# Optimization experiments

Hardware: AMD Instinct MI355X
Metric: run time of the kernel (lower is better)

Reference implementation:

```python
import jax, jax.numpy as jnp
import numpy as np

H, DQS, DQP, DVS, DVP = 12, 16, 4, 16, 8
S_SCALAR = (3.0 * DQS) ** -0.5
S_POINT = (3.0 * DQP * (9.0 * 2.0 ** 0.5)) ** -0.5
S_PAIR = 3.0 ** -0.5
_OFF = np.cumsum([0, H * DQS, H * DQS, H * DVS, H * DQP * 3, H * DQP * 3, H * DVP * 3])


def _ln(x, g, b, eps=1e-5):
    mu = x.mean(-1, keepdims=True)
    var = x.var(-1, keepdims=True)
    return (x - mu) / jnp.sqrt(var + eps) * g + b


def setup_inputs() -> dict:
    B, N, D, PD = 2, 512, 384, 128
    key = jax.random.key(0)
    ks = jax.random.split(key, 12)
    node_feats = jax.random.normal(ks[0], (B, N, D), jnp.float32)
    pair_feats = jax.random.normal(ks[1], (B, N, N, PD), jnp.float32)
    mask = jnp.ones((B, N), dtype=bool)
    # random per-residue rigid frames (orthonormal rotations via QR)
    rot = jnp.linalg.qr(jax.random.normal(ks[2], (B, N, 3, 3), jnp.float32))[0]
    trans = jax.random.normal(ks[3], (B, N, 3), jnp.float32)
    dim_qkv = int(_OFF[-1])             # 1152
    dim_out = H * (PD + DVS + 4 * DVP)  # 2112
    s = 0.02
    p = dict(
        ln_s_g=jnp.ones((D,)), ln_s_b=jnp.zeros((D,)),
        ln_p_g=jnp.ones((PD,)), ln_p_b=jnp.zeros((PD,)),
        w_pair_bias=s * jax.random.normal(ks[4], (PD, H), jnp.float32),
        w_qkv=s * jax.random.normal(ks[5], (D, dim_qkv), jnp.float32),
        point_weights=jnp.full((1, H, 1, 1), float(np.log(np.e - 1.0)), jnp.float32),
        w_out=s * jax.random.normal(ks[6], (dim_out, D), jnp.float32),
        b_out=jnp.zeros((D,)),
        ln_t_g=jnp.ones((D,)), ln_t_b=jnp.zeros((D,)),
        w_ff1=s * jax.random.normal(ks[7], (D, 4 * D), jnp.float32),
        b_ff1=jnp.zeros((4 * D,)),
        w_ff2=s * jax.random.normal(ks[8], (4 * D, D), jnp.float32),
        b_ff2=jnp.zeros((D,)),
    )
    return dict(node_feats=node_feats, pair_feats=pair_feats, mask=mask,
                rot=rot, trans=trans, **p)


def reference(node_feats, pair_feats, mask, rot, trans,
              ln_s_g, ln_s_b, ln_p_g, ln_p_b, w_pair_bias, w_qkv,
              point_weights, w_out, b_out,
              ln_t_g, ln_t_b, w_ff1, b_ff1, w_ff2, b_ff2):
    b, n, d = node_feats.shape
    x = _ln(node_feats, ln_s_g, ln_s_b)
    p = _ln(pair_feats, ln_p_g, ln_p_b)
    pair_bias = jnp.einsum('bijd,dh->bhij', p, w_pair_bias)
    qkv = x @ w_qkv  # (b,n,1152)

    def heads(t, dh):
        return t.reshape(b, n, H, dh).transpose(0, 2, 1, 3)  # b h n d

    q_s = heads(qkv[..., _OFF[0]:_OFF[1]], DQS)
    k_s = heads(qkv[..., _OFF[1]:_OFF[2]], DQS)
    v_s = heads(qkv[..., _OFF[2]:_OFF[3]], DVS)

    def to_pts(t, dp):
        pts = t.reshape(b, n, H * dp, 3)
        # rigid apply: R_i @ x + t_i (global frame)
        pts = jnp.einsum('bnxy,bnpy->bnpx', rot, pts) + trans[:, :, None, :]
        return pts.reshape(b, n, H, dp, 3).transpose(0, 2, 1, 3, 4)  # b h n d 3

    q_p = to_pts(qkv[..., _OFF[3]:_OFF[4]], DQP)
    k_p = to_pts(qkv[..., _OFF[4]:_OFF[5]], DQP)
    v_p = to_pts(qkv[..., _OFF[5]:_OFF[6]], DVP)

    scalar_logits = jnp.einsum('bhid,bhjd->bhij', q_s, k_s)
    # dist attn: -sum_{d,c} (q-k)^2, expanded to avoid (b,h,n,n,d,3) intermediate
    qq = jnp.sum(q_p * q_p, axis=(-1, -2))
    kk = jnp.sum(k_p * k_p, axis=(-1, -2))
    qk = jnp.einsum('bhidc,bhjdc->bhij', q_p, k_p)
    point_logits = -(qq[..., :, None] + kk[..., None, :] - 2.0 * qk)
    point_logits = point_logits * jax.nn.softplus(point_weights)

    neg = jnp.finfo(node_feats.dtype).min
    pm = mask[:, None, :, None] & mask[:, None, None, :]  # b 1 i j
    scalar_logits = jnp.where(pm, scalar_logits, neg)
    point_logits = jnp.where(pm, point_logits, neg)
    pair_bias = jnp.where(pm, pair_bias, neg)

    logits = S_SCALAR * scalar_logits + S_POINT * point_logits + S_PAIR * pair_bias
    attn = jax.nn.softmax(logits, axis=-1)

    out_s = jnp.einsum('bhij,bhjd->bhid', attn, v_s)
    out_pair = jnp.einsum('bhij,bijd->bhid', attn, p)
    out_p = jnp.einsum('bhij,bhjdc->bhidc', attn, v_p)
    # rigid inverse: R_i^T (x - t_i) back to local frame
    pts = out_p.transpose(0, 2, 1, 3, 4).reshape(b, n, H * DVP, 3)
    pts = jnp.einsum('bnyx,bnpy->bnpx', rot, pts - trans[:, :, None, :])
    out_p = pts.reshape(b, n, H, DVP, 3)
    pnorm = jnp.sqrt(jnp.sum(out_p * out_p, axis=-1) + 1e-8)  # safe_norm

    cat = jnp.concatenate([
        out_s.transpose(0, 2, 1, 3).reshape(b, n, H * DVS),
        out_p.reshape(b, n, H * DVP * 3),
        pnorm.reshape(b, n, H * DVP),
        out_pair.transpose(0, 2, 1, 3).reshape(b, n, -1),
    ], axis=-1)
    attn_out = cat @ w_out + b_out

    # residuals + transition (dropout=0 -> identity). Note: transition is
    # applied to attn_out (pre-residual), exactly as in the torch forward.
    node1 = attn_out + node_feats
    t = _ln(attn_out, ln_t_g, ln_t_b)
    t = jax.nn.gelu(t @ w_ff1 + b_ff1) @ w_ff2 + b_ff2
    return t + node1
```

## Files before the change

### kernel.cpp

```cpp
#include <hip/hip_runtime.h>
#include <hip/hip_bf16.h>
#include <math.h>

typedef __hip_bfloat16 bf16;
typedef _Float16 f16;
typedef unsigned short ushort_t;
typedef ushort_t ushort8 __attribute__((ext_vector_type(8)));
typedef ushort_t us4 __attribute__((ext_vector_type(4)));
typedef short bf16x8 __attribute__((ext_vector_type(8)));
typedef f16 f16x8 __attribute__((ext_vector_type(8)));
typedef float f32x4 __attribute__((ext_vector_type(4)));

constexpr float S_SCALAR = 0.14433756729740643f;
constexpr float S_POINT  = 0.08091531528f;
constexpr float S_PAIR   = 0.5773502691896258f;

__device__ inline short f2bfs(float x) {
  return (short)__builtin_bit_cast(unsigned short, __float2bfloat16(x));
}
__device__ inline ushort_t f2bfu(float x) {
  return (ushort_t)__builtin_bit_cast(unsigned short, __float2bfloat16(x));
}
__device__ inline ushort_t f2hu(float x) {
  return __builtin_bit_cast(ushort_t, (f16)x);
}
__device__ inline float h2f(ushort_t u) {
  return (float)__builtin_bit_cast(f16, u);
}

__device__ inline float gelu_tanh(float x) {
  float c = 0.7978845608028654f * (x + 0.044715f * x * x * x);
  return 0.5f * x * (1.f + tanhf(c));
}

__global__ __launch_bounds__(128) void ln384_kernel(
    const float* __restrict__ in, const float* __restrict__ g,
    const float* __restrict__ b, float* __restrict__ out)
{
  int row = blockIdx.x;
  const float* x = in + (size_t)row * 384;
  int t = threadIdx.x;
  float v[3]; float s = 0.f, s2 = 0.f;
#pragma unroll
  for (int i = 0; i < 3; i++) { v[i] = x[t + 128 * i]; s += v[i]; s2 += v[i] * v[i]; }
  for (int o = 32; o; o >>= 1) { s += __shfl_down(s, o); s2 += __shfl_down(s2, o); }
  __shared__ float sh[4];
  int wid = t >> 6, lane = t & 63;
  if (lane == 0) { sh[wid] = s; sh[2 + wid] = s2; }
  __syncthreads();
  s = sh[0] + sh[1]; s2 = sh[2] + sh[3];
  float mean = s * (1.f / 384.f);
  float var = s2 * (1.f / 384.f) - mean * mean;
  float rstd = rsqrtf(fmaxf(var, 0.f) + 1e-5f);
  float* orow = out + (size_t)row * 384;
#pragma unroll
  for (int i = 0; i < 3; i++) {
    int c = t + 128 * i;
    orow[c] = (v[i] - mean) * rstd * g[c] + b[c];
  }
}

__global__ __launch_bounds__(256) void prep_all_kernel(
    const float* __restrict__ w_qkv, const float* __restrict__ w_out,
    const float* __restrict__ w_ff1, const float* __restrict__ w_ff2,
    ushort_t* __restrict__ wqkvT, ushort_t* __restrict__ woutT,
    ushort_t* __restrict__ wff1T, ushort_t* __restrict__ wff2T,
    const float* __restrict__ g, const float* __restrict__ bb,
    const float* __restrict__ wpb, ushort_t* __restrict__ gwbT,
    float* __restrict__ gsbs,
    const float* __restrict__ node, const float* __restrict__ ln_s_g,
    const float* __restrict__ ln_s_b, float* __restrict__ xout)
{
  __shared__ float shmem[2048];
  int bid = blockIdx.x;
  int t = threadIdx.x;
  if (bid < 2376) {
    const float* src; ushort_t* dst; int K, N, bx, by;
    if (bid < 432)       { src = w_qkv; dst = wqkvT; K = 384;  N = 1152; bx = bid % 36;          by = bid / 36; }
    else if (bid < 1224) { src = w_out; dst = woutT; K = 2112; N = 384;  bx = (bid - 432) % 12;  by = (bid - 432) / 12; }
    else if (bid < 1800) { src = w_ff1; dst = wff1T; K = 384;  N = 1536; bx = (bid - 1224) % 48; by = (bid - 1224) / 48; }
    else                 { src = w_ff2; dst = wff2T; K = 1536; N = 384;  bx = (bid - 1800) % 12; by = (bid - 1800) / 12; }
    float (&tile)[32][33] = *reinterpret_cast<float (*)[32][33]>(shmem);
    int n0 = bx * 32, k0 = by * 32;
    int c = t & 31, r4 = (t >> 5) * 4;
#pragma unroll
    for (int i = 0; i < 4; i++)
      tile[r4 + i][c] = src[(size_t)(k0 + r4 + i) * N + n0 + c];
    __syncthreads();
#pragma unroll
    for (int i = 0; i < 4; i++)
      dst[(size_t)(n0 + r4 + i) * K + k0 + c] = f2bfu(tile[c][r4 + i]);
    return;
  }
  if (bid == 2376) {
    for (int idx = t; idx < 2048; idx += 256) {
      int h = idx >> 7, c = idx & 127;
      float v = (h < 12) ? g[c] * wpb[c * 12 + h] : 0.f;
      bf16 r = __float2bfloat16(v);
      gwbT[idx] = __builtin_bit_cast(unsigned short, r);
      shmem[idx] = __bfloat162float(r);
    }
    __syncthreads();
    if (t < 16) {
      float s = 0.f;
      for (int c = 0; c < 128; c++) s += shmem[t * 128 + c];
      gsbs[t] = s;
    } else if (t < 32) {
      int h = t - 16;
      float s = 0.f;
      if (h < 12) for (int c = 0; c < 128; c++) s = fmaf(bb[c], wpb[c * 12 + h], s);
// ... 76 lines not shown
      acc[1][1] = __builtin_amdgcn_mfma_f32_16x16x32_bf16(af1, bf1, acc[1][1], 0, 0, 0);
    }
    __syncthreads();
  }
#pragma unroll
  for (int mf = 0; mf < 2; mf++) {
#pragma unroll
    for (int nf = 0; nf < 2; nf++) {
      int nn = n0 + wn + nf * 16 + lr;
      float bv = bias ? bias[nn] : 0.f;
#pragma unroll
      for (int e = 0; e < 4; e++) {
        int m = m0 + wm + mf * 16 + lk * 4 + e;
        float v = acc[mf][nf][e] + bv;
        if (EPI == 1) v = gelu_tanh(v);
        if (EPI == 2) v += r1[(size_t)m * Nn + nn] + r2[(size_t)m * Nn + nn];
        C[(size_t)m * Nn + nn] = v;
      }
    }
  }
}

template <int EPI>
__global__ __launch_bounds__(256) void gemm_mfma_m32_kernel(
    const float* __restrict__ A, const ushort_t* __restrict__ BT,
    const float* __restrict__ bias, const float* __restrict__ r1,
    const float* __restrict__ r2, float* __restrict__ C,
    int M, int Nn, int K)
{
  __shared__ ushort_t As[32][72];
  __shared__ ushort_t Bs[64][72];
  int t = threadIdx.x;
  int w = t >> 6, l = t & 63;
  int m0 = blockIdx.y * 32, n0 = blockIdx.x * 64;
  int wm = (w & 1) * 16, wn = (w >> 1) * 32;
  int lr = l & 15, lk = l >> 4;
  int ar = t >> 3, ac = (t & 7) * 8;
  int br = t >> 2, bc = (t & 3) * 16;
  f32x4 acc[2];
  acc[0] = (f32x4){0.f, 0.f, 0.f, 0.f};
  acc[1] = (f32x4){0.f, 0.f, 0.f, 0.f};

  for (int k0 = 0; k0 < K; k0 += 64) {
    const float* Ar = A + (size_t)(m0 + ar) * K + k0 + ac;
    float4 a0 = *(const float4*)(Ar + 0);
    float4 a1 = *(const float4*)(Ar + 4);
    ushort8 u;
    u[0] = f2bfu(a0.x); u[1] = f2bfu(a0.y); u[2] = f2bfu(a0.z); u[3] = f2bfu(a0.w);
    u[4] = f2bfu(a1.x); u[5] = f2bfu(a1.y); u[6] = f2bfu(a1.z); u[7] = f2bfu(a1.w);
    *(ushort8*)&As[ar][ac] = u;
    const ushort_t* Br = BT + (size_t)(n0 + br) * K + k0 + bc;
    *(ushort8*)&Bs[br][bc] = *(const ushort8*)(Br + 0);
    *(ushort8*)&Bs[br][bc + 8] = *(const ushort8*)(Br + 8);
    __syncthreads();
#pragma unroll
    for (int kk = 0; kk < 2; kk++) {
      bf16x8 af = *(const bf16x8*)&As[wm + lr][kk * 32 + lk * 8];
      bf16x8 bf0 = *(const bf16x8*)&Bs[wn + lr][kk * 32 + lk * 8];
      bf16x8 bf1 = *(const bf16x8*)&Bs[wn + 16 + lr][kk * 32 + lk * 8];
      acc[0] = __builtin_amdgcn_mfma_f32_16x16x32_bf16(af, bf0, acc[0], 0, 0, 0);
      acc[1] = __builtin_amdgcn_mfma_f32_16x16x32_bf16(af, bf1, acc[1], 0, 0, 0);
    }
    __syncthreads();
  }
#pragma unroll
  for (int nf = 0; nf < 2; nf++) {
    int nn = n0 + wn + nf * 16 + lr;
    float bv = bias ? bias[nn] : 0.f;
#pragma unroll
    for (int e = 0; e < 4; e++) {
      int m = m0 + wm + lk * 4 + e;
      float v = acc[nf][e] + bv;
      if (EPI == 1) v = gelu_tanh(v);
      if (EPI == 2) v += r1[(size_t)m * Nn + nn] + r2[(size_t)m * Nn + nn];
      C[(size_t)m * Nn + nn] = v;
    }
  }
}

__global__ __launch_bounds__(256) void qkv_post_kernel(
    const float* __restrict__ qkv, const float* __restrict__ rot,
    const float* __restrict__ trans, const float* __restrict__ pw,
    f16* __restrict__ qhat, f16* __restrict__ khat,
    float* __restrict__ kkb, ushort_t* __restrict__ vT)
{
  int bh = blockIdx.x;
  int b = bh / 12, h = bh - b * 12;
  int role = blockIdx.y >> 1;
  int j = (blockIdx.y & 1) * 256 + threadIdx.x;
  int bn = b * 512 + j;
  const float* row = qkv + (size_t)bn * 1152;
  float R[9];
#pragma unroll
  for (int k = 0; k < 9; k++) R[k] = rot[bn * 9 + k];
  float T0 = trans[bn * 3], T1 = trans[bn * 3 + 1], T2 = trans[bn * 3 + 2];
  if (role == 0) {
    float sp = log1pf(__expf(pw[h]));
    float c1 = 2.f * S_POINT * sp;
    f16* qh = qhat + ((size_t)bh * 512 + j) * 32;
#pragma unroll
    for (int d = 0; d < 16; d++) qh[d] = (f16)(S_SCALAR * row[h * 16 + d]);
#pragma unroll
    for (int p = 0; p < 4; p++) {
      int base = 576 + (h * 4 + p) * 3;
      float x = row[base], y = row[base + 1], z = row[base + 2];
      qh[16 + p * 3 + 0] = (f16)(c1 * (R[0] * x + R[1] * y + R[2] * z + T0));
      qh[16 + p * 3 + 1] = (f16)(c1 * (R[3] * x + R[4] * y + R[5] * z + T1));
      qh[16 + p * 3 + 2] = (f16)(c1 * (R[6] * x + R[7] * y + R[8] * z + T2));
    }
#pragma unroll
    for (int d = 28; d < 32; d++) qh[d] = (f16)0.f;
  } else if (role == 1) {
    f16* kh = khat + ((size_t)bh * 512 + j) * 32;
#pragma unroll
    for (int d = 0; d < 16; d++) kh[d] = (f16)(row[192 + h * 16 + d]);
    float kksum = 0.f;
#pragma unroll
    for (int p = 0; p < 4; p++) {
      int base = 720 + (h * 4 + p) * 3;
      float x = row[base], y = row[base + 1], z = row[base + 2];
      float gx = R[0] * x + R[1] * y + R[2] * z + T0;
      float gy = R[3] * x + R[4] * y + R[5] * z + T1;
      float gz = R[6] * x + R[7] * y + R[8] * z + T2;
      kh[16 + p * 3 + 0] = (f16)gx; kh[16 + p * 3 + 1] = (f16)gy; kh[16 + p * 3 + 2] = (f16)gz;
      kksum = fmaf(gx, gx, kksum); kksum = fmaf(gy, gy, kksum); kksum = fmaf(gz, gz, kksum);
    }
#pragma unroll
    for (int d = 28; d < 32; d++) kh[d] = (f16)0.f;
    kkb[(size_t)bh * 512 + j] = kksum;
  } else {
    ushort_t* vt = vT + (size_t)bh * 40 * 512;
#pragma unroll
    for (int c = 0; c < 16; c++) vt[c * 512 + j] = f2hu(row[384 + h * 16 + c]);
#pragma unroll
    for (int p = 0; p < 8; p++) {
      int base = 864 + (h * 8 + p) * 3;
      float x = row[base], y = row[base + 1], z = row[base + 2];
      vt[(16 + p * 3 + 0) * 512 + j] = f2hu(R[0] * x + R[1] * y + R[2] * z + T0);
      vt[(16 + p * 3 + 1) * 512 + j] = f2hu(R[3] * x + R[4] * y + R[5] * z + T1);
      vt[(16 + p * 3 + 2) * 512 + j] = f2hu(R[6] * x + R[7] * y + R[8] * z + T2);
    }
  }
}

__global__ __launch_bounds__(256) void pair_bias_kernel(
    const float* __restrict__ pair, const ushort_t* __restrict__ gwbT,
    const float* __restrict__ gsbs, const float* __restrict__ g,
    const float* __restrict__ bb, ushort_t* __restrict__ bias,
    f16* __restrict__ pnT)
{
  __shared__ ushort_t tile[128][136];
  int t = threadIdx.x;
  int wv = t >> 6, l = t & 63;
  int lr = l & 15, lk = l >> 4;
  size_t rid0 = (size_t)blockIdx.x * 128 + (size_t)wv * 32;

  bf16x8 bfrag[4];
#pragma unroll
  for (int kc = 0; kc < 4; kc++) {
    const ushort_t* gp = gwbT + lr * 128 + kc * 32 + lk * 8;
    us4 q0 = *(const us4*)gp;
    us4 q1 = *(const us4*)(gp + 4);
    bfrag[kc][0] = (short)q0[0]; bfrag[kc][1] = (short)q0[1];
    bfrag[kc][2] = (short)q0[2]; bfrag[kc][3] = (short)q0[3];
    bfrag[kc][4] = (short)q1[0]; bfrag[kc][5] = (short)q1[1];
    bfrag[kc][6] = (short)q1[2]; bfrag[kc][7] = (short)q1[3];
  }

  const float* p0 = pair + (rid0 + lr) * 128 + lk * 8;
  f32x4 acc0 = {0.f, 0.f, 0.f, 0.f}, acc1 = {0.f, 0.f, 0.f, 0.f};
  float s0 = 0.f, s20 = 0.f, s1 = 0.f, s21 = 0.f;
#pragma unroll
  for (int kc = 0; kc < 4; kc++) {
    float4 u0 = *(const float4*)(p0 + kc * 32);
    float4 u1 = *(const float4*)(p0 + kc * 32 + 4);
    float4 w0 = *(const float4*)(p0 + 2048 + kc * 32);
    float4 w1 = *(const float4*)(p0 + 2048 + kc * 32 + 4);
    s0 += u0.x + u0.y + u0.z + u0.w + u1.x + u1.y + u1.z + u1.w;
    s20 = fmaf(u0.x, u0.x, s20); s20 = fmaf(u0.y, u0.y, s20);
    s20 = fmaf(u0.z, u0.z, s20); s20 = fmaf(u0.w, u0.w, s20);
    s20 = fmaf(u1.x, u1.x, s20); s20 = fmaf(u1.y, u1.y, s20);
    s20 = fmaf(u1.z, u1.z, s20); s20 = fmaf(u1.w, u1.w, s20);
    s1 += w0.x + w0.y + w0.z + w0.w + w1.x + w1.y + w1.z + w1.w;
    s21 = fmaf(w0.x, w0.x, s21); s21 = fmaf(w0.y, w0.y, s21);
    s21 = fmaf(w0.z, w0.z, s21); s21 = fmaf(w0.w, w0.w, s21);
    s21 = fmaf(w1.x, w1.x, s21); s21 = fmaf(w1.y, w1.y, s21);
    s21 = fmaf(w1.z, w1.z, s21); s21 = fmaf(w1.w, w1.w, s21);
    bf16x8 a0, a1;
    a0[0] = f2bfs(u0.x); a0[1] = f2bfs(u0.y); a0[2] = f2bfs(u0.z); a0[3] = f2bfs(u0.w);
    a0[4] = f2bfs(u1.x); a0[5] = f2bfs(u1.y); a0[6] = f2bfs(u1.z); a0[7] = f2bfs(u1.w);
    a1[0] = f2bfs(w0.x); a1[1] = f2bfs(w0.y); a1[2] = f2bfs(w0.z); a1[3] = f2bfs(w0.w);
    a1[4] = f2bfs(w1.x); a1[5] = f2bfs(w1.y); a1[6] = f2bfs(w1.z); a1[7] = f2bfs(w1.w);
    acc0 = __builtin_amdgcn_mfma_f32_16x16x32_bf16(a0, bfrag[kc], acc0, 0, 0, 0);
    acc1 = __builtin_amdgcn_mfma_f32_16x16x32_bf16(a1, bfrag[kc], acc1, 0, 0, 0);
  }
  s0 += __shfl_xor(s0, 16);  s0 += __shfl_xor(s0, 32);
  s20 += __shfl_xor(s20, 16); s20 += __shfl_xor(s20, 32);
  s1 += __shfl_xor(s1, 16);  s1 += __shfl_xor(s1, 32);
  s21 += __shfl_xor(s21, 16); s21 += __shfl_xor(s21, 32);
  float mean0 = s0 * (1.f / 128.f);
  float rstd0 = rsqrtf(fmaxf(s20 * (1.f / 128.f) - mean0 * mean0, 0.f) + 1e-5f);
  float mean1 = s1 * (1.f / 128.f);
  float rstd1 = rsqrtf(fmaxf(s21 * (1.f / 128.f) - mean1 * mean1, 0.f) + 1e-5f);

  int jl_u = wv * 32 + lr, jl_w = wv * 32 + 16 + lr;
#pragma unroll
  for (int kc = 0; kc < 4; kc++) {
    int c0 = kc * 32 + lk * 8;
    float4 u0 = *(const float4*)(p0 + kc * 32);
    float4 u1 = *(const float4*)(p0 + kc * 32 + 4);
    float4 w0 = *(const float4*)(p0 + 2048 + kc * 32);
    float4 w1 = *(const float4*)(p0 + 2048 + kc * 32 + 4);
    float4 g0 = *(const float4*)(g + c0);
    float4 g1 = *(const float4*)(g + c0 + 4);
    float4 b0 = *(const float4*)(bb + c0);
    float4 b1 = *(const float4*)(bb + c0 + 4);
    float uu[8] = {u0.x, u0.y, u0.z, u0.w, u1.x, u1.y, u1.z, u1.w};
    float ww[8] = {w0.x, w0.y, w0.z, w0.w, w1.x, w1.y, w1.z, w1.w};
    float gg[8] = {g0.x, g0.y, g0.z, g0.w, g1.x, g1.y, g1.z, g1.w};
    float bv[8] = {b0.x, b0.y, b0.z, b0.w, b1.x, b1.y, b1.z, b1.w};
#pragma unroll
    for (int e = 0; e < 8; e++) {
      int c = c0 + e;
      int sw = ((c >> 3) & 7) << 4;
      tile[c][jl_u ^ sw] = f2hu(fmaf((uu[e] - mean0) * rstd0, gg[e], bv[e]));
      tile[c][jl_w ^ sw] = f2hu(fmaf((ww[e] - mean1) * rstd1, gg[e], bv[e]));
    }
  }
  __syncthreads();
  {
    int slab = blockIdx.x >> 2;
    int j0blk = (blockIdx.x & 3) * 128;
    ushort_t* dstb = (ushort_t*)pnT + (size_t)slab * 65536 + j0blk;
#pragma unroll
    for (int it = 0; it < 8; it++) {
      int idx = t + 256 * it;
      int c = idx >> 4, o = idx & 15;
      int sw = ((c >> 3) & 7) << 4;
      ushort8 v = *(const ushort8*)&tile[c][(o * 8) ^ sw];
      *(ushort8*)(dstb + (size_t)c * 512 + o * 8) = v;
    }
  }

  float gsum = gsbs[lr], bsum = gsbs[16 + lr];
  int b = (int)(rid0 >> 18);
  int i = (int)((rid0 >> 9) & 511);
  int j0 = (int)(rid0 & 511);
  us4 pk0, pk1;
#pragma unroll
  for (int e = 0; e < 4; e++) {
    int r = lk * 4 + e;
    float m0 = __shfl(mean0, r), rs0 = __shfl(rstd0, r);
    float m1 = __shfl(mean1, r), rs1 = __shfl(rstd1, r);
    pk0[e] = f2hu(rs0 * (acc0[e] - m0 * gsum) + bsum);
    pk1[e] = f2hu(rs1 * (acc1[e] - m1 * gsum) + bsum);
  }
  if (lr < 12) {
    ushort_t* dst = bias + ((size_t)(b * 12 + lr) * 512 + i) * 512 + j0 + lk * 4;
    *(us4*)dst = pk0;
    *(us4*)(dst + 16) = pk1;
  }
}

__global__ __launch_bounds__(256, 1) void attn_kernel(
    const f16* __restrict__ qhat, const f16* __restrict__ khat,
    const float* __restrict__ kkb, const ushort_t* __restrict__ bias,
    const float* __restrict__ pw, ushort_t* __restrict__ attn)
{
  int i0 = blockIdx.x * 64;
  int bh = blockIdx.y;
  int b = bh / 12, h = bh - b * 12;
  int t = threadIdx.x;
  int w = t >> 6, l = t & 63, lr = l & 15, lk = l >> 4;
  float spp = S_POINT * log1pf(__expf(pw[h]));
  int i = i0 + w * 16 + lr;
  f16x8 bfrag = *(const f16x8*)(qhat + ((size_t)bh * 512 + i) * 32 + lk * 8);
  const f16* kbase = khat + (size_t)bh * 512 * 32;
  const float* kkrow = kkb + (size_t)bh * 512;
  const ushort_t* brow = bias + ((size_t)bh * 512 + i) * 512;
  float lg[32][4];
  float pmax = -3.0e38f;
#pragma unroll
  for (int jt = 0; jt < 32; jt++) {
    f16x8 afrag = *(const f16x8*)(kbase + (size_t)(jt * 16 + lr) * 32 + lk * 8);
    f32x4 c = {0.f, 0.f, 0.f, 0.f};
    c = __builtin_amdgcn_mfma_f32_16x16x32_f16(afrag, bfrag, c, 0, 0, 0);
    us4 bq = *(const us4*)(brow + jt * 16 + lk * 4);
    float4 kq = *(const float4*)(kkrow + jt * 16 + lk * 4);
    float kk4[4] = {kq.x, kq.y, kq.z, kq.w};
#pragma unroll
    for (int e = 0; e < 4; e++) {
      float lv = c[e] + S_PAIR * h2f(bq[e]) - spp * kk4[e];
      lg[jt][e] = lv;
      pmax = fmaxf(pmax, lv);
    }
  }
  pmax = fmaxf(pmax, __shfl_xor(pmax, 16));
  pmax = fmaxf(pmax, __shfl_xor(pmax, 32));
  float ssum = 0.f;
#pragma unroll
  for (int jt = 0; jt < 32; jt++)
#pragma unroll
    for (int e = 0; e < 4; e++) {
      float p = __expf(lg[jt][e] - pmax);
      lg[jt][e] = p;
      ssum += p;
    }
  ssum += __shfl_xor(ssum, 16);
  ssum += __shfl_xor(ssum, 32);
  float inv = 1.f / ssum;
  ushort_t* arow = attn + ((size_t)(b * 512 + i) * 12 + h) * 512;
#pragma unroll
  for (int jt = 0; jt < 32; jt++) {
    us4 o;
#pragma unroll
    for (int e = 0; e < 4; e++) o[e] = f2hu(lg[jt][e] * inv);
    *(us4*)(arow + jt * 16 + lk * 4) = o;
  }
}

__global__ __launch_bounds__(256) void sv_gemm_kernel(
    const ushort_t* __restrict__ attn, const ushort_t* __restrict__ vT,
    float* __restrict__ svraw)
{
  int i0 = blockIdx.x * 64;
  int bh = blockIdx.y;
  int b = bh / 12, h = bh - b * 12;
  __shared__ ushort_t As_[64][72];
  __shared__ ushort_t Bs_[48][72];
  int t = threadIdx.x;
  int w = t >> 6, l = t & 63, lr = l & 15, lk = l >> 4;
  int ai = t >> 2, as = (t & 3) * 16;
  const ushort_t* vbase = vT + (size_t)bh * 40 * 512;
  f32x4 acc[3];
#pragma unroll
  for (int n = 0; n < 3; n++) acc[n] = (f32x4){0.f, 0.f, 0.f, 0.f};

  for (int jt = 0; jt < 8; jt++) {
    int jb = jt * 64;
    size_t aoff = ((size_t)(b * 512 + i0 + ai) * 12 + h) * 512 + jb + as;
    ushort8 a0 = *(const ushort8*)(attn + aoff);
    ushort8 a1 = *(const ushort8*)(attn + aoff + 8);
    *(ushort8*)&As_[ai][as] = a0;
    *(ushort8*)&As_[ai][as + 8] = a1;
    for (int idx = t; idx < 384; idx += 256) {
      int c = idx >> 3, j8 = (idx & 7) * 8;
      ushort8 v = {0, 0, 0, 0, 0, 0, 0, 0};
      if (c < 40) v = *(const ushort8*)(vbase + (size_t)c * 512 + jb + j8);
      *(ushort8*)&Bs_[c][j8] = v;
    }
    __syncthreads();
#pragma unroll
    for (int kk = 0; kk < 2; kk++) {
      f16x8 af = *(const f16x8*)&As_[w * 16 + lr][kk * 32 + lk * 8];
#pragma unroll
      for (int n = 0; n < 3; n++) {
        f16x8 bf_ = *(const f16x8*)&Bs_[n * 16 + lr][kk * 32 + lk * 8];
        acc[n] = __builtin_amdgcn_mfma_f32_16x16x32_f16(af, bf_, acc[n], 0, 0, 0);
      }
    }
    __syncthreads();
  }
#pragma unroll
  for (int n = 0; n < 3; n++) {
    int c = n * 16 + lr;
    if (c < 40) {
#pragma unroll
      for (int e = 0; e < 4; e++) {
        int i = i0 + w * 16 + lk * 4 + e;
        svraw[(size_t)(b * 512 + i) * 480 + h * 40 + c] = acc[n][e];
      }
    }
  }
}

__global__ __launch_bounds__(256) void pair_out_kernel(
    const ushort_t* __restrict__ attn, const f16* __restrict__ pnT,
    const float* __restrict__ svraw, const float* __restrict__ rot,
    const float* __restrict__ trans, float* __restrict__ cat)
{
  int bn = blockIdx.x;
  int t = threadIdx.x;
  const float* sv = svraw + (size_t)bn * 480;
  float* crow = cat + (size_t)bn * 2112;
  if (t < 192) {
    int h2 = t >> 4, d = t & 15;
    crow[t] = sv[h2 * 40 + d];
    if (t < 96) {
      int h3 = t >> 3, dp = t & 7;
      float T0 = trans[bn * 3], T1 = trans[bn * 3 + 1], T2 = trans[bn * 3 + 2];
      const float* R = rot + bn * 9;
      float px = sv[h3 * 40 + 16 + dp * 3 + 0] - T0;
      float py = sv[h3 * 40 + 16 + dp * 3 + 1] - T1;
      float pz = sv[h3 * 40 + 16 + dp * 3 + 2] - T2;
      float lx = R[0] * px + R[3] * py + R[6] * pz;
      float ly = R[1] * px + R[4] * py + R[7] * pz;
      float lz = R[2] * px + R[5] * py + R[8] * pz;
      crow[192 + h3 * 24 + dp * 3 + 0] = lx;
      crow[192 + h3 * 24 + dp * 3 + 1] = ly;
      crow[192 + h3 * 24 + dp * 3 + 2] = lz;
      crow[480 + h3 * 8 + dp] = sqrtf(lx * lx + ly * ly + lz * lz + 1e-8f);
    }
  }
  int w = t >> 6, l = t & 63, lr = l & 15, lk = l >> 4;
  const ushort_t* arow = attn + (size_t)bn * 12 * 512;
  int ar = (lr < 12) ? lr : 11;
  const f16* slab = pnT + (size_t)bn * 65536;
  int n0 = w * 32;
  f32x4 acc0 = {0.f, 0.f, 0.f, 0.f}, acc1 = {0.f, 0.f, 0.f, 0.f};
#pragma unroll
  for (int ks = 0; ks < 16; ks++) {
    int kb = ks * 32 + lk * 8;
    f16x8 af = *(const f16x8*)((const f16*)arow + (size_t)ar * 512 + kb);
    f16x8 b0 = *(const f16x8*)(slab + (size_t)(n0 + lr) * 512 + kb);
    f16x8 b1 = *(const f16x8*)(slab + (size_t)(n0 + 16 + lr) * 512 + kb);
    acc0 = __builtin_amdgcn_mfma_f32_16x16x32_f16(af, b0, acc0, 0, 0, 0);
    acc1 = __builtin_amdgcn_mfma_f32_16x16x32_f16(af, b1, acc1, 0, 0, 0);
  }
#pragma unroll
  for (int e = 0; e < 4; e++) {
    int hh = lk * 4 + e;
    if (hh < 12) {
      crow[576 + hh * 128 + n0 + lr] = acc0[e];
      crow[576 + hh * 128 + n0 + 16 + lr] = acc1[e];
    }
  }
}

extern "C" void kernel_launch(void* const* d_in, const int* in_sizes, int n_in,
                              void* d_out, int out_size, void* d_ws, size_t ws_size,
                              hipStream_t stream)
{
  const float* node   = (const float*)d_in[0];
  const float* pair   = (const float*)d_in[1];
  const float* rot    = (const float*)d_in[3];
  const float* trans  = (const float*)d_in[4];
  const float* ln_s_g = (const float*)d_in[5];
  const float* ln_s_b = (const float*)d_in[6];
  const float* ln_p_g = (const float*)d_in[7];
  const float* ln_p_b = (const float*)d_in[8];
  const float* wpb    = (const float*)d_in[9];
  const float* w_qkv  = (const float*)d_in[10];
  const float* pw     = (const float*)d_in[11];
  const float* w_out  = (const float*)d_in[12];
  const float* b_out  = (const float*)d_in[13];
  const float* ln_t_g = (const float*)d_in[14];
  const float* ln_t_b = (const float*)d_in[15];
  const float* w_ff1  = (const float*)d_in[16];
  const float* b_ff1  = (const float*)d_in[17];
  const float* w_ff2  = (const float*)d_in[18];
  const float* b_ff2  = (const float*)d_in[19];
  float* out = (float*)d_out;
  float* ws = (float*)d_ws;

  float* qkv    = ws;
  float* x      = ws + 1179648;
  float* tn     = x;
  float* ao     = ws + 1572864;
  float* svraw  = ws + 1966080;
  ushort_t* biasb = (ushort_t*)(ws + 2457600);
  float* cat    = ws + 2457600;
  ushort_t* attnb = (ushort_t*)(ws + 5603328);
  float* gb     = ws + 5603328;
  ushort_t* gwbT = (ushort_t*)(ws + 8749056);
  float* gsbs   = ws + 8750080;
  ushort_t* wqkvT = (ushort_t*)(ws + 8750112);
  ushort_t* woutT = (ushort_t*)(ws + 8971296);
  ushort_t* wff1T = (ushort_t*)(ws + 9376800);
  ushort_t* wff2T = (ushort_t*)(ws + 9671712);
  f16* qhat     = (f16*)(ws + 9966624);
  f16* khat     = (f16*)(ws + 10163232);
  float* kkb    = ws + 10359840;
  ushort_t* vT  = (ushort_t*)(ws + 10372128);
  f16* pnT      = (f16*)(ws + 10617888);

  prep_all_kernel<<<2889, 256, 0, stream>>>(w_qkv, w_out, w_ff1, w_ff2,
      wqkvT, woutT, wff1T, wff2T, ln_p_g, ln_p_b, wpb, gwbT, gsbs,
      node, ln_s_g, ln_s_b, x);
  gemm_mfma_kernel<0><<<dim3(18, 16), 256, 0, stream>>>(x, wqkvT, nullptr, nullptr, nullptr, qkv, 1024, 1152, 384);
  qkv_post_kernel<<<dim3(24, 6), 256, 0, stream>>>(qkv, rot, trans, pw, qhat, khat, kkb, vT);
  pair_bias_kernel<<<4096, 256, 0, stream>>>(pair, gwbT, gsbs, ln_p_g, ln_p_b, biasb, pnT);
  attn_kernel<<<dim3(8, 24), 256, 0, stream>>>(qhat, khat, kkb, biasb, pw, attnb);
  sv_gemm_kernel<<<dim3(8, 24), 256, 0, stream>>>(attnb, vT, svraw);
  pair_out_kernel<<<1024, 256, 0, stream>>>(attnb, pnT, svraw, rot, trans, cat);
  gemm_mfma_m32_kernel<0><<<dim3(6, 32), 256, 0, stream>>>(cat, woutT, b_out, nullptr, nullptr, ao, 1024, 384, 2112);
  ln384_kernel<<<1024, 128, 0, stream>>>(ao, ln_t_g, ln_t_b, tn);
  gemm_mfma_kernel<1><<<dim3(24, 16), 256, 0, stream>>>(tn, wff1T, b_ff1, nullptr, nullptr, gb, 1024, 1536, 384);
  gemm_mfma_m32_kernel<2><<<dim3(6, 32), 256, 0, stream>>>(gb, wff2T, b_ff2, ao, node, out, 1024, 384, 1536);
}
```

Measured before the change: 587.6 us.

## Fuse pair LayerNorm, pair bias, softmax and pair-output into one per-row kernel

Replaces the pair_bias, attention and pair_out kernels with a single kernel per (b,i) row. It layer-normalises the pair slab, computes the bias with MFMA, does the q·k logits with fdot2 and an online softmax over four 128-column chunks, then accumulates attn·pair from shared memory. The -spp·|k|² term is folded into qhat/khat as an extra dot-product element, so the kkb buffer goes away. This avoids writing and re-reading the bias and the transposed normalized pair tensor (pnT) in global memory. In exchange it adds many block-wide syncs per chunk and stores |k|² in fp16, which risks precision loss.

```diff
diff --git a/kernel.cpp b/kernel.cpp
--- a/kernel.cpp
+++ b/kernel.cpp
@@ -9,7 +9,9 @@
 typedef ushort_t us4 __attribute__((ext_vector_type(4)));
 typedef short bf16x8 __attribute__((ext_vector_type(8)));
 typedef f16 f16x8 __attribute__((ext_vector_type(8)));
+typedef f16 f16x2 __attribute__((ext_vector_type(2)));
 typedef float f32x4 __attribute__((ext_vector_type(4)));
+typedef unsigned int u32x4 __attribute__((ext_vector_type(4)));
 
 constexpr float S_SCALAR = 0.14433756729740643f;
 constexpr float S_POINT  = 0.08091531528f;
@@ -26,6 +28,15 @@
 }
 __device__ inline float h2f(ushort_t u) {
   return (float)__builtin_bit_cast(f16, u);
+}
+__device__ inline float fdot2f(unsigned a, unsigned b, float c) {
+#if __has_builtin(__builtin_amdgcn_fdot2)
+  return __builtin_amdgcn_fdot2(__builtin_bit_cast(f16x2, a),
+                                __builtin_bit_cast(f16x2, b), c, false);
+#else
+  f16x2 av = __builtin_bit_cast(f16x2, a), bv = __builtin_bit_cast(f16x2, b);
+  return c + (float)av[0] * (float)bv[0] + (float)av[1] * (float)bv[1];
+#endif
 }
 
 __device__ inline float gelu_tanh(float x) {
@@ -268,7 +279,7 @@
     const float* __restrict__ qkv, const float* __restrict__ rot,
     const float* __restrict__ trans, const float* __restrict__ pw,
     f16* __restrict__ qhat, f16* __restrict__ khat,
-    float* __restrict__ kkb, ushort_t* __restrict__ vT)
+    ushort_t* __restrict__ vT)
 {
   int bh = blockIdx.x;
   int b = bh / 12, h = bh - b * 12;
@@ -283,6 +294,7 @@
   if (role == 0) {
     float sp = log1pf(__expf(pw[h]));
     float c1 = 2.f * S_POINT * sp;
+    float spp = S_POINT * sp;
     f16* qh = qhat + ((size_t)bh * 512 + j) * 32;
 #pragma unroll
     for (int d = 0; d < 16; d++) qh[d] = (f16)(S_SCALAR * row[h * 16 + d]);
@@ -294,8 +306,8 @@
       qh[16 + p * 3 + 1] = (f16)(c1 * (R[3] * x + R[4] * y + R[5] * z + T1));
       qh[16 + p * 3 + 2] = (f16)(c1 * (R[6] * x + R[7] * y + R[8] * z + T2));
     }
-#pragma unroll
-    for (int d = 28; d < 32; d++) qh[d] = (f16)0.f;
+    qh[28] = (f16)(-spp);
+    qh[29] = (f16)0.f; qh[30] = (f16)0.f; qh[31] = (f16)0.f;
   } else if (role == 1) {
     f16* kh = khat + ((size_t)bh * 512 + j) * 32;
 #pragma unroll
@@ -311,9 +323,8 @@
       kh[16 + p * 3 + 0] = (f16)gx; kh[16 + p * 3 + 1] = (f16)gy; kh[16 + p * 3 + 2] = (f16)gz;
       kksum = fmaf(gx, gx, kksum); kksum = fmaf(gy, gy, kksum); kksum = fmaf(gz, gz, kksum);
     }
-#pragma unroll
-    for (int d = 28; d < 32; d++) kh[d] = (f16)0.f;
-    kkb[(size_t)bh * 512 + j] = kksum;
+    kh[28] = (f16)kksum;
+    kh[29] = (f16)0.f; kh[30] = (f16)0.f; kh[31] = (f16)0.f;
   } else {
     ushort_t* vt = vT + (size_t)bh * 40 * 512;
 #pragma unroll
@@ -329,18 +340,32 @@
   }
 }
 
-__global__ __launch_bounds__(256) void pair_bias_kernel(
+__global__ __launch_bounds__(256) void mega_kernel(
     const float* __restrict__ pair, const ushort_t* __restrict__ gwbT,
     const float* __restrict__ gsbs, const float* __restrict__ g,
-    const float* __restrict__ bb, ushort_t* __restrict__ bias,
-    f16* __restrict__ pnT)
+    const float* __restrict__ bb, const f16* __restrict__ qhat,
+    const f16* __restrict__ khat, ushort_t* __restrict__ attnb,
+    float* __restrict__ cat)
 {
   __shared__ ushort_t tile[128][136];
+  __shared__ ushort_t Ps[16][520];
+  __shared__ ushort_t bias_s[16][136];
+  __shared__ unsigned qhat_u[12][16];
+  __shared__ float red_s[2][6][4];
+  __shared__ float m_s[16], l_s[16], r_s[16], invl_s[16];
+  __shared__ float mhist_s[4][16], cf_s[4][16];
+
+  int bn = blockIdx.x;
+  int b = bn >> 9, i = bn & 511;
   int t = threadIdx.x;
-  int wv = t >> 6, l = t & 63;
-  int lr = l & 15, lk = l >> 4;
-  size_t rid0 = (size_t)blockIdx.x * 128 + (size_t)wv * 32;
-
+  int wv = t >> 6, ln = t & 63, lr = ln & 15, lk = ln >> 4;
+
+  if (t < 16) { m_s[t] = -3.0e38f; l_s[t] = 0.f; r_s[t] = 1.f; }
+  for (int idx = t; idx < 4 * 520; idx += 256) Ps[12 + idx / 520][idx % 520] = 0;
+  if (t < 192) {
+    int h = t >> 4, d4 = t & 15;
+    qhat_u[h][d4] = ((const unsigned*)qhat)[((size_t)(b * 12 + h) * 512 + i) * 16 + d4];
+  }
   bf16x8 bfrag[4];
 #pragma unroll
   for (int kc = 0; kc < 4; kc++) {
@@ -352,156 +377,180 @@
     bfrag[kc][4] = (short)q1[0]; bfrag[kc][5] = (short)q1[1];
     bfrag[kc][6] = (short)q1[2]; bfrag[kc][7] = (short)q1[3];
   }
-
-  const float* p0 = pair + (rid0 + lr) * 128 + lk * 8;
-  f32x4 acc0 = {0.f, 0.f, 0.f, 0.f}, acc1 = {0.f, 0.f, 0.f, 0.f};
-  float s0 = 0.f, s20 = 0.f, s1 = 0.f, s21 = 0.f;
-#pragma unroll
-  for (int kc = 0; kc < 4; kc++) {
-    float4 u0 = *(const float4*)(p0 + kc * 32);
-    float4 u1 = *(const float4*)(p0 + kc * 32 + 4);
-    float4 w0 = *(const float4*)(p0 + 2048 + kc * 32);
-    float4 w1 = *(const float4*)(p0 + 2048 + kc * 32 + 4);
-    s0 += u0.x + u0.y + u0.z + u0.w + u1.x + u1.y + u1.z + u1.w;
-    s20 = fmaf(u0.x, u0.x, s20); s20 = fmaf(u0.y, u0.y, s20);
-    s20 = fmaf(u0.z, u0.z, s20); s20 = fmaf(u0.w, u0.w, s20);
-    s20 = fmaf(u1.x, u1.x, s20); s20 = fmaf(u1.y, u1.y, s20);
-    s20 = fmaf(u1.z, u1.z, s20); s20 = fmaf(u1.w, u1.w, s20);
-    s1 += w0.x + w0.y + w0.z + w0.w + w1.x + w1.y + w1.z + w1.w;
-    s21 = fmaf(w0.x, w0.x, s21); s21 = fmaf(w0.y, w0.y, s21);
-    s21 = fmaf(w0.z, w0.z, s21); s21 = fmaf(w0.w, w0.w, s21);
-    s21 = fmaf(w1.x, w1.x, s21); s21 = fmaf(w1.y, w1.y, s21);
-    s21 = fmaf(w1.z, w1.z, s21); s21 = fmaf(w1.w, w1.w, s21);
-    bf16x8 a0, a1;
-    a0[0] = f2bfs(u0.x); a0[1] = f2bfs(u0.y); a0[2] = f2bfs(u0.z); a0[3] = f2bfs(u0.w);
-    a0[4] = f2bfs(u1.x); a0[5] = f2bfs(u1.y); a0[6] = f2bfs(u1.z); a0[7] = f2bfs(u1.w);
-    a1[0] = f2bfs(w0.x); a1[1] = f2bfs(w0.y); a1[2] = f2bfs(w0.z); a1[3] = f2bfs(w0.w);
-    a1[4] = f2bfs(w1.x); a1[5] = f2bfs(w1.y); a1[6] = f2bfs(w1.z); a1[7] = f2bfs(w1.w);
-    acc0 = __builtin_amdgcn_mfma_f32_16x16x32_bf16(a0, bfrag[kc], acc0, 0, 0, 0);
-    acc1 = __builtin_amdgcn_mfma_f32_16x16x32_bf16(a1, bfrag[kc], acc1, 0, 0, 0);
-  }
-  s0 += __shfl_xor(s0, 16);  s0 += __shfl_xor(s0, 32);
-  s20 += __shfl_xor(s20, 16); s20 += __shfl_xor(s20, 32);
-  s1 += __shfl_xor(s1, 16);  s1 += __shfl_xor(s1, 32);
-  s21 += __shfl_xor(s21, 16); s21 += __shfl_xor(s21, 32);
-  float mean0 = s0 * (1.f / 128.f);
-  float rstd0 = rsqrtf(fmaxf(s20 * (1.f / 128.f) - mean0 * mean0, 0.f) + 1e-5f);
-  float mean1 = s1 * (1.f / 128.f);
-  float rstd1 = rsqrtf(fmaxf(s21 * (1.f / 128.f) - mean1 * mean1, 0.f) + 1e-5f);
-
-  int jl_u = wv * 32 + lr, jl_w = wv * 32 + 16 + lr;
-#pragma unroll
-  for (int kc = 0; kc < 4; kc++) {
-    int c0 = kc * 32 + lk * 8;
-    float4 u0 = *(const float4*)(p0 + kc * 32);
-    float4 u1 = *(const float4*)(p0 + kc * 32 + 4);
-    float4 w0 = *(const float4*)(p0 + 2048 + kc * 32);
-    float4 w1 = *(const float4*)(p0 + 2048 + kc * 32 + 4);
-    float4 g0 = *(const float4*)(g + c0);
-    float4 g1 = *(const float4*)(g + c0 + 4);
-    float4 b0 = *(const float4*)(bb + c0);
-    float4 b1 = *(const float4*)(bb + c0 + 4);
-    float uu[8] = {u0.x, u0.y, u0.z, u0.w, u1.x, u1.y, u1.z, u1.w};
-    float ww[8] = {w0.x, w0.y, w0.z, w0.w, w1.x, w1.y, w1.z, w1.w};
-    float gg[8] = {g0.x, g0.y, g0.z, g0.w, g1.x, g1.y, g1.z, g1.w};
-    float bv[8] = {b0.x, b0.y, b0.z, b0.w, b1.x, b1.y, b1.z, b1.w};
-#pragma unroll
-    for (int e = 0; e < 8; e++) {
-      int c = c0 + e;
-      int sw = ((c >> 3) & 7) << 4;
-      tile[c][jl_u ^ sw] = f2hu(fmaf((uu[e] - mean0) * rstd0, gg[e], bv[e]));
-      tile[c][jl_w ^ sw] = f2hu(fmaf((ww[e] - mean1) * rstd1, gg[e], bv[e]));
-    }
-  }
+  float gsum = gsbs[lr];
+  float bsP = S_PAIR * gsbs[16 + lr];
+  int n0 = wv * 32;
+  int sw0 = (((n0 + lr) >> 3) & 7) << 4;
+  int sw1 = (((n0 + 16 + lr) >> 3) & 7) << 4;
+  f32x4 po0 = {0.f, 0.f, 0.f, 0.f}, po1 = {0.f, 0.f, 0.f, 0.f};
   __syncthreads();
-  {
-    int slab = blockIdx.x >> 2;
-    int j0blk = (blockIdx.x & 3) * 128;
-    ushort_t* dstb = (ushort_t*)pnT + (size_t)slab * 65536 + j0blk;
-#pragma unroll
-    for (int it = 0; it < 8; it++) {
-      int idx = t + 256 * it;
-      int c = idx >> 4, o = idx & 15;
-      int sw = ((c >> 3) & 7) << 4;
-      ushort8 v = *(const ushort8*)&tile[c][(o * 8) ^ sw];
-      *(ushort8*)(dstb + (size_t)c * 512 + o * 8) = v;
-    }
-  }
-
-  float gsum = gsbs[lr], bsum = gsbs[16 + lr];
-  int b = (int)(rid0 >> 18);
-  int i = (int)((rid0 >> 9) & 511);
-  int j0 = (int)(rid0 & 511);
-  us4 pk0, pk1;
+
+  for (int ck = 0; ck < 4; ck++) {
+    int jc = ck * 128;
+    const float* p0 = pair + ((size_t)bn * 512 + jc + wv * 32 + lr) * 128 + lk * 8;
+    f32x4 acc0 = {0.f, 0.f, 0.f, 0.f}, acc1 = {0.f, 0.f, 0.f, 0.f};
+    float s0 = 0.f, s20 = 0.f, s1 = 0.f, s21 = 0.f;
+#pragma unroll
+    for (int kc = 0; kc < 4; kc++) {
+      float4 u0 = *(const float4*)(p0 + kc * 32);
+      float4 u1 = *(const float4*)(p0 + kc * 32 + 4);
+      float4 w0 = *(const float4*)(p0 + 2048 + kc * 32);
+      float4 w1 = *(const float4*)(p0 + 2048 + kc * 32 + 4);
+      s0 += u0.x + u0.y + u0.z + u0.w + u1.x + u1.y + u1.z + u1.w;
+      s20 = fmaf(u0.x, u0.x, s20); s20 = fmaf(u0.y, u0.y, s20);
+      s20 = fmaf(u0.z, u0.z, s20); s20 = fmaf(u0.w, u0.w, s20);
+      s20 = fmaf(u1.x, u1.x, s20); s20 = fmaf(u1.y, u1.y, s20);
+      s20 = fmaf(u1.z, u1.z, s20); s20 = fmaf(u1.w, u1.w, s20);
+      s1 += w0.x + w0.y + w0.z + w0.w + w1.x + w1.y + w1.z + w1.w;
+      s21 = fmaf(w0.x, w0.x, s21); s21 = fmaf(w0.y, w0.y, s21);
+      s21 = fmaf(w0.z, w0.z, s21); s21 = fmaf(w0.w, w0.w, s21);
+      s21 = fmaf(w1.x, w1.x, s21); s21 = fmaf(w1.y, w1.y, s21);
+      s21 = fmaf(w1.z, w1.z, s21); s21 = fmaf(w1.w, w1.w, s21);
+      bf16x8 a0, a1;
+      a0[0] = f2bfs(u0.x); a0[1] = f2bfs(u0.y); a0[2] = f2bfs(u0.z); a0[3] = f2bfs(u0.w);
+      a0[4] = f2bfs(u1.x); a0[5] = f2bfs(u1.y); a0[6] = f2bfs(u1.z); a0[7] = f2bfs(u1.w);
+      a1[0] = f2bfs(w0.x); a1[1] = f2bfs(w0.y); a1[2] = f2bfs(w0.z); a1[3] = f2bfs(w0.w);
+      a1[4] = f2bfs(w1.x); a1[5] = f2bfs(w1.y); a1[6] = f2bfs(w1.z); a1[7] = f2bfs(w1.w);
+      acc0 = __builtin_amdgcn_mfma_f32_16x16x32_bf16(a0, bfrag[kc], acc0, 0, 0, 0);
+      acc1 = __builtin_amdgcn_mfma_f32_16x16x32_bf16(a1, bfrag[kc], acc1, 0, 0, 0);
+    }
+    s0 += __shfl_xor(s0, 16);  s0 += __shfl_xor(s0, 32);
+    s20 += __shfl_xor(s20, 16); s20 += __shfl_xor(s20, 32);
+    s1 += __shfl_xor(s1, 16);  s1 += __shfl_xor(s1, 32);
+    s21 += __shfl_xor(s21, 16); s21 += __shfl_xor(s21, 32);
+    float mean0 = s0 * (1.f / 128.f);
+    float rstd0 = rsqrtf(fmaxf(s20 * (1.f / 128.f) - mean0 * mean0, 0.f) + 1e-5f);
+    float mean1 = s1 * (1.f / 128.f);
+    float rstd1 = rsqrtf(fmaxf(s21 * (1.f / 128.f) - mean1 * mean1, 0.f) + 1e-5f);
+    int jl_u = wv * 32 + lr, jl_w = wv * 32 + 16 + lr;
+#pragma unroll
+    for (int kc = 0; kc < 4; kc++) {
+      int c0 = kc * 32 + lk * 8;
+      float4 u0 = *(const float4*)(p0 + kc * 32);
+      float4 u1 = *(const float4*)(p0 + kc * 32 + 4);
+      float4 w0 = *(const float4*)(p0 + 2048 + kc * 32);
+      float4 w1 = *(const float4*)(p0 + 2048 + kc * 32 + 4);
+      float4 g0 = *(const float4*)(g + c0);
+      float4 g1 = *(const float4*)(g + c0 + 4);
+      float4 b0 = *(const float4*)(bb + c0);
+      float4 b1 = *(const float4*)(bb + c0 + 4);
+      float uu[8] = {u0.x, u0.y, u0.z, u0.w, u1.x, u1.y, u1.z, u1.w};
+      float ww[8] = {w0.x, w0.y, w0.z, w0.w, w1.x, w1.y, w1.z, w1.w};
+      float gg[8] = {g0.x, g0.y, g0.z, g0.w, g1.x, g1.y, g1.z, g1.w};
+      float bv[8] = {b0.x, b0.y, b0.z, b0.w, b1.x, b1.y, b1.z, b1.w};
+#pragma unroll
+      for (int e = 0; e < 8; e++) {
+        int c = c0 + e;
+        int sw = ((c >> 3) & 7) << 4;
+        tile[c][jl_u ^ sw] = f2hu(fmaf((uu[e] - mean0) * rstd0, gg[e], bv[e]));
+        tile[c][jl_w ^ sw] = f2hu(fmaf((ww[e] - mean1) * rstd1, gg[e], bv[e]));
+      }
+    }
+    {
+      us4 pk0, pk1;
+#pragma unroll
+      for (int e = 0; e < 4; e++) {
+        int r = lk * 4 + e;
+        float m0 = __shfl(mean0, r), rs0 = __shfl(rstd0, r);
+        float m1 = __shfl(mean1, r), rs1 = __shfl(rstd1, r);
+        pk0[e] = f2hu(fmaf(S_PAIR * rs0, acc0[e] - m0 * gsum, bsP));
+        pk1[e] = f2hu(fmaf(S_PAIR * rs1, acc1[e] - m1 * gsum, bsP));
+      }
+      *(us4*)&bias_s[lr][wv * 32 + lk * 4] = pk0;
+      *(us4*)&bias_s[lr][wv * 32 + 16 + lk * 4] = pk1;
+    }
+    __syncthreads();
+    float lgv[6];
+#pragma unroll
+    for (int q = 0; q < 6; q++) {
+      int h = 2 * q + (wv >> 1);
+      int jl = (wv & 1) * 64 + ln;
+      const u32x4* kr = (const u32x4*)(khat + ((size_t)(b * 12 + h) * 512 + jc + jl) * 32);
+      float d = 0.f;
+#pragma unroll
+      for (int qq = 0; qq < 4; qq++) {
+        u32x4 kv = kr[qq];
+        u32x4 qv = *(const u32x4*)&qhat_u[h][qq * 4];
+        d = fdot2f(kv[0], qv[0], d);
+        d = fdot2f(kv[1], qv[1], d);
+        d = fdot2f(kv[2], qv[2], d);
+        d = fdot2f(kv[3], qv[3], d);
+      }
+      lgv[q] = d + h2f(bias_s[h][jl]);
+    }
+#pragma unroll
+    for (int q = 0; q < 6; q++) {
+      float m = lgv[q];
+      m = fmaxf(m, __shfl_xor(m, 1));  m = fmaxf(m, __shfl_xor(m, 2));
+      m = fmaxf(m, __shfl_xor(m, 4));  m = fmaxf(m, __shfl_xor(m, 8));
+      m = fmaxf(m, __shfl_xor(m, 16)); m = fmaxf(m, __shfl_xor(m, 32));
+      if (ln == 0) red_s[0][q][wv] = m;
+    }
+    __syncthreads();
+    if (t < 12) {
+      int q = t >> 1, wp = (t & 1) * 2;
+      float cm = fmaxf(red_s[0][q][wp], red_s[0][q][wp + 1]);
+      float mo = m_s[t];
+      float mn = fmaxf(mo, cm);
+      m_s[t] = mn; r_s[t] = __expf(mo - mn); mhist_s[ck][t] = mn;
+    }
+    __syncthreads();
+#pragma unroll
+    for (int q = 0; q < 6; q++) {
+      int h = 2 * q + (wv >> 1);
+      int jl = (wv & 1) * 64 + ln;
+      float p = __expf(lgv[q] - m_s[h]);
+      Ps[h][jc + jl] = f2hu(p);
+      float s = p;
+      s += __shfl_xor(s, 1);  s += __shfl_xor(s, 2);
+      s += __shfl_xor(s, 4);  s += __shfl_xor(s, 8);
+      s += __shfl_xor(s, 16); s += __shfl_xor(s, 32);
+      if (ln == 0) red_s[1][q][wv] = s;
+    }
+#pragma unroll
+    for (int e = 0; e < 4; e++) {
+      float rr = r_s[lk * 4 + e];
+      po0[e] *= rr; po1[e] *= rr;
+    }
+    __syncthreads();
+    if (t < 12) {
+      int q = t >> 1, wp = (t & 1) * 2;
+      l_s[t] = l_s[t] * r_s[t] + red_s[1][q][wp] + red_s[1][q][wp + 1];
+    }
+#pragma unroll
+    for (int ks = 0; ks < 4; ks++) {
+      int kb = ks * 32 + lk * 8;
+      f16x8 af = *(const f16x8*)&Ps[lr][jc + kb];
+      f16x8 b0 = *(const f16x8*)&tile[n0 + lr][kb ^ sw0];
+      f16x8 b1 = *(const f16x8*)&tile[n0 + 16 + lr][kb ^ sw1];
+      po0 = __builtin_amdgcn_mfma_f32_16x16x32_f16(af, b0, po0, 0, 0, 0);
+      po1 = __builtin_amdgcn_mfma_f32_16x16x32_f16(af, b1, po1, 0, 0, 0);
+    }
+    __syncthreads();
+  }
+  if (t < 64) {
+    int c = t >> 4, h = t & 15;
+    cf_s[c][h] = __expf(mhist_s[c][h] - m_s[h]);
+  }
+  if (t < 16) invl_s[t] = 1.f / l_s[t];
+  __syncthreads();
+  ushort_t* arow = attnb + (size_t)bn * 12 * 512;
+#pragma unroll
+  for (int it = 0; it < 24; it++) {
+    int idx = t + 256 * it;
+    int h = idx >> 9, j = idx & 511;
+    float v = h2f(Ps[h][j]) * cf_s[j >> 7][h] * invl_s[h];
+    arow[(size_t)h * 512 + j] = f2hu(v);
+  }
+  float* crow = cat + (size_t)bn * 2112 + 576;
 #pragma unroll
   for (int e = 0; e < 4; e++) {
-    int r = lk * 4 + e;
-    float m0 = __shfl(mean0, r), rs0 = __shfl(rstd0, r);
-    float m1 = __shfl(mean1, r), rs1 = __shfl(rstd1, r);
-    pk0[e] = f2hu(rs0 * (acc0[e] - m0 * gsum) + bsum);
-    pk1[e] = f2hu(rs1 * (acc1[e] - m1 * gsum) + bsum);
-  }
-  if (lr < 12) {
-    ushort_t* dst = bias + ((size_t)(b * 12 + lr) * 512 + i) * 512 + j0 + lk * 4;
-    *(us4*)dst = pk0;
-    *(us4*)(dst + 16) = pk1;
-  }
-}
-
-__global__ __launch_bounds__(256, 1) void attn_kernel(
-    const f16* __restrict__ qhat, const f16* __restrict__ khat,
-    const float* __restrict__ kkb, const ushort_t* __restrict__ bias,
-    const float* __restrict__ pw, ushort_t* __restrict__ attn)
-{
-  int i0 = blockIdx.x * 64;
-  int bh = blockIdx.y;
-  int b = bh / 12, h = bh - b * 12;
-  int t = threadIdx.x;
-  int w = t >> 6, l = t & 63, lr = l & 15, lk = l >> 4;
-  float spp = S_POINT * log1pf(__expf(pw[h]));
-  int i = i0 + w * 16 + lr;
-  f16x8 bfrag = *(const f16x8*)(qhat + ((size_t)bh * 512 + i) * 32 + lk * 8);
-  const f16* kbase = khat + (size_t)bh * 512 * 32;
-  const float* kkrow = kkb + (size_t)bh * 512;
-  const ushort_t* brow = bias + ((size_t)bh * 512 + i) * 512;
-  float lg[32][4];
-  float pmax = -3.0e38f;
-#pragma unroll
-  for (int jt = 0; jt < 32; jt++) {
-    f16x8 afrag = *(const f16x8*)(kbase + (size_t)(jt * 16 + lr) * 32 + lk * 8);
-    f32x4 c = {0.f, 0.f, 0.f, 0.f};
-    c = __builtin_amdgcn_mfma_f32_16x16x32_f16(afrag, bfrag, c, 0, 0, 0);
-    us4 bq = *(const us4*)(brow + jt * 16 + lk * 4);
-    float4 kq = *(const float4*)(kkrow + jt * 16 + lk * 4);
-    float kk4[4] = {kq.x, kq.y, kq.z, kq.w};
-#pragma unroll
-    for (int e = 0; e < 4; e++) {
-      float lv = c[e] + S_PAIR * h2f(bq[e]) - spp * kk4[e];
-      lg[jt][e] = lv;
-      pmax = fmaxf(pmax, lv);
-    }
-  }
-  pmax = fmaxf(pmax, __shfl_xor(pmax, 16));
-  pmax = fmaxf(pmax, __shfl_xor(pmax, 32));
-  float ssum = 0.f;
-#pragma unroll
-  for (int jt = 0; jt < 32; jt++)
-#pragma unroll
-    for (int e = 0; e < 4; e++) {
-      float p = __expf(lg[jt][e] - pmax);
-      lg[jt][e] = p;
-      ssum += p;
-    }
-  ssum += __shfl_xor(ssum, 16);
-  ssum += __shfl_xor(ssum, 32);
-  float inv = 1.f / ssum;
-  ushort_t* arow = attn + ((size_t)(b * 512 + i) * 12 + h) * 512;
-#pragma unroll
-  for (int jt = 0; jt < 32; jt++) {
-    us4 o;
-#pragma unroll
-    for (int e = 0; e < 4; e++) o[e] = f2hu(lg[jt][e] * inv);
-    *(us4*)(arow + jt * 16 + lk * 4) = o;
+    int hh = lk * 4 + e;
+    if (hh < 12) {
+      float il = invl_s[hh];
+      crow[hh * 128 + n0 + lr] = po0[e] * il;
+      crow[hh * 128 + n0 + 16 + lr] = po1[e] * il;
+    }
   }
 }
 
@@ -560,56 +609,32 @@
   }
 }
 
-__global__ __launch_bounds__(256) void pair_out_kernel(
-    const ushort_t* __restrict__ attn, const f16* __restrict__ pnT,
+__global__ __launch_bounds__(192) void sv_epilogue_kernel(
     const float* __restrict__ svraw, const float* __restrict__ rot,
     const float* __restrict__ trans, float* __restrict__ cat)
 {
   int bn = blockIdx.x;
-  int t = threadIdx.x;
   const float* sv = svraw + (size_t)bn * 480;
   float* crow = cat + (size_t)bn * 2112;
-  if (t < 192) {
+  int t = threadIdx.x;
+  {
     int h2 = t >> 4, d = t & 15;
     crow[t] = sv[h2 * 40 + d];
-    if (t < 96) {
-      int h3 = t >> 3, dp = t & 7;
-      float T0 = trans[bn * 3], T1 = trans[bn * 3 + 1], T2 = trans[bn * 3 + 2];
-      const float* R = rot + bn * 9;
-      float px = sv[h3 * 40 + 16 + dp * 3 + 0] - T0;
-      float py = sv[h3 * 40 + 16 + dp * 3 + 1] - T1;
-      float pz = sv[h3 * 40 + 16 + dp * 3 + 2] - T2;
-      float lx = R[0] * px + R[3] * py + R[6] * pz;
-      float ly = R[1] * px + R[4] * py + R[7] * pz;
-      float lz = R[2] * px + R[5] * py + R[8] * pz;
-      crow[192 + h3 * 24 + dp * 3 + 0] = lx;
-      crow[192 + h3 * 24 + dp * 3 + 1] = ly;
-      crow[192 + h3 * 24 + dp * 3 + 2] = lz;
-      crow[480 + h3 * 8 + dp] = sqrtf(lx * lx + ly * ly + lz * lz + 1e-8f);
-    }
-  }
-  int w = t >> 6, l = t & 63, lr = l & 15, lk = l >> 4;
-  const ushort_t* arow = attn + (size_t)bn * 12 * 512;
-  int ar = (lr < 12) ? lr : 11;
-  const f16* slab = pnT + (size_t)bn * 65536;
-  int n0 = w * 32;
-  f32x4 acc0 = {0.f, 0.f, 0.f, 0.f}, acc1 = {0.f, 0.f, 0.f, 0.f};
-#pragma unroll
-  for (int ks = 0; ks < 16; ks++) {
-    int kb = ks * 32 + lk * 8;
-    f16x8 af = *(const f16x8*)((const f16*)arow + (size_t)ar * 512 + kb);
-    f16x8 b0 = *(const f16x8*)(slab + (size_t)(n0 + lr) * 512 + kb);
-    f16x8 b1 = *(const f16x8*)(slab + (size_t)(n0 + 16 + lr) * 512 + kb);
-    acc0 = __builtin_amdgcn_mfma_f32_16x16x32_f16(af, b0, acc0, 0, 0, 0);
-    acc1 = __builtin_amdgcn_mfma_f32_16x16x32_f16(af, b1, acc1, 0, 0, 0);
-  }
-#pragma unroll
-  for (int e = 0; e < 4; e++) {
-    int hh = lk * 4 + e;
-    if (hh < 12) {
-      crow[576 + hh * 128 + n0 + lr] = acc0[e];
-      crow[576 + hh * 128 + n0 + 16 + lr] = acc1[e];
-    }
+  }
+  if (t < 96) {
+    int h2 = t >> 3, dp = t & 7;
+    float T0 = trans[bn * 3], T1 = trans[bn * 3 + 1], T2 = trans[bn * 3 + 2];
+    const float* R = rot + bn * 9;
+    float px = sv[h2 * 40 + 16 + dp * 3 + 0] - T0;
+    float py = sv[h2 * 40 + 16 + dp * 3 + 1] - T1;
+    float pz = sv[h2 * 40 + 16 + dp * 3 + 2] - T2;
+    float lx = R[0] * px + R[3] * py + R[6] * pz;
+    float ly = R[1] * px + R[4] * py + R[7] * pz;
+    float lz = R[2] * px + R[5] * py + R[8] * pz;
+    crow[192 + h2 * 24 + dp * 3 + 0] = lx;
+    crow[192 + h2 * 24 + dp * 3 + 1] = ly;
+    crow[192 + h2 * 24 + dp * 3 + 2] = lz;
+    crow[480 + h2 * 8 + dp] = sqrtf(lx * lx + ly * ly + lz * lz + 1e-8f);
   }
 }
 
@@ -644,7 +669,6 @@
   float* tn     = x;
   float* ao     = ws + 1572864;
   float* svraw  = ws + 1966080;
-  ushort_t* biasb = (ushort_t*)(ws + 2457600);
   float* cat    = ws + 2457600;
   ushort_t* attnb = (ushort_t*)(ws + 5603328);
   float* gb     = ws + 5603328;
@@ -656,19 +680,16 @@
   ushort_t* wff2T = (ushort_t*)(ws + 9671712);
   f16* qhat     = (f16*)(ws + 9966624);
   f16* khat     = (f16*)(ws + 10163232);
-  float* kkb    = ws + 10359840;
-  ushort_t* vT  = (ushort_t*)(ws + 10372128);
-  f16* pnT      = (f16*)(ws + 10617888);
+  ushort_t* vT  = (ushort_t*)(ws + 10359840);
 
   prep_all_kernel<<<2889, 256, 0, stream>>>(w_qkv, w_out, w_ff1, w_ff2,
       wqkvT, woutT, wff1T, wff2T, ln_p_g, ln_p_b, wpb, gwbT, gsbs,
       node, ln_s_g, ln_s_b, x);
   gemm_mfma_kernel<0><<<dim3(18, 16), 256, 0, stream>>>(x, wqkvT, nullptr, nullptr, nullptr, qkv, 1024, 1152, 384);
-  qkv_post_kernel<<<dim3(24, 6), 256, 0, stream>>>(qkv, rot, trans, pw, qhat, khat, kkb, vT);
-  pair_bias_kernel<<<4096, 256, 0, stream>>>(pair, gwbT, gsbs, ln_p_g, ln_p_b, biasb, pnT);
-  attn_kernel<<<dim3(8, 24), 256, 0, stream>>>(qhat, khat, kkb, biasb, pw, attnb);
+  qkv_post_kernel<<<dim3(24, 6), 256, 0, stream>>>(qkv, rot, trans, pw, qhat, khat, vT);
+  mega_kernel<<<1024, 256, 0, stream>>>(pair, gwbT, gsbs, ln_p_g, ln_p_b, qhat, khat, attnb, cat);
   sv_gemm_kernel<<<dim3(8, 24), 256, 0, stream>>>(attnb, vT, svraw);
-  pair_out_kernel<<<1024, 256, 0, stream>>>(attnb, pnT, svraw, rot, trans, cat);
+  sv_epilogue_kernel<<<1024, 192, 0, stream>>>(svraw, rot, trans, cat);
   gemm_mfma_m32_kernel<0><<<dim3(6, 32), 256, 0, stream>>>(cat, woutT, b_out, nullptr, nullptr, ao, 1024, 384, 2112);
   ln384_kernel<<<1024, 128, 0, stream>>>(ao, ln_t_g, ln_t_b, tn);
   gemm_mfma_kernel<1><<<dim3(24, 16), 256, 0, stream>>>(tn, wff1T, b_ff1, nullptr, nullptr, gb, 1024, 1536, 384);
```

Result: slower. 606.3 us (+3.2%).
